# Kernel optimization log

Measured on AMD Instinct MI355X. Metric: run time of the kernel, lower is better.

Reference implementation:

```python
import jax, jax.numpy as jnp
import numpy as np

B, C, L = 8, 512, 2048


def setup_inputs() -> dict:
    key = jax.random.key(0)
    ks = jax.random.split(key, 7)
    s = 1.0 / np.sqrt(C)
    return {
        "x": jax.random.normal(ks[0], (B, C, L), dtype=jnp.float32),
        "Wq": jax.random.normal(ks[1], (C, C), dtype=jnp.float32) * s,
        "bq": jax.random.normal(ks[2], (C,), dtype=jnp.float32) * s,
        "Wk": jax.random.normal(ks[3], (C, C), dtype=jnp.float32) * s,
        "bk": jax.random.normal(ks[4], (C,), dtype=jnp.float32) * s,
        "Wv": jax.random.normal(ks[5], (C, C), dtype=jnp.float32) * s,
        "bv": jax.random.normal(ks[6], (C,), dtype=jnp.float32) * s,
    }


def reference(x, Wq, bq, Wk, bk, Wv, bv):
    # Conv1d(kernel_size=1) == per-position linear: [C_out, C_in] @ x[b,:,l]
    q = jnp.einsum('oi,bil->bol', Wq, x) + bq[None, :, None]  # [B, C, L]
    k = jnp.einsum('oi,bil->bol', Wk, x) + bk[None, :, None]
    v = jnp.einsum('oi,bil->bol', Wv, x) + bv[None, :, None]
    scale = 1.0 / jnp.sqrt(jnp.asarray(x.shape[1], dtype=x.dtype))
    # scores[b, l, m] = sum_c q[b,c,l] * k[b,c,m] / sqrt(C)
    scores = jnp.einsum('bcl,bcm->blm', q, k) * scale  # [B, L, L]
    attn = jax.nn.softmax(scores, axis=-1)
    # out[b, c, l] = sum_m v[b,c,m] * attn[b,l,m]   (== bmm(V, attn^T))
    return jnp.einsum('bcm,blm->bcl', v, attn)  # [B, C, L]
```

## Files before the change

### kernel.cpp

```cpp
#include <hip/hip_runtime.h>
#include <hip/hip_bf16.h>
#include <math.h>

#define B 8
#define C 512
#define L 2048

using bf16x8 = __bf16 __attribute__((ext_vector_type(8)));
using f32x4  = float __attribute__((ext_vector_type(4)));

#define MFMA(a, b, c) __builtin_amdgcn_mfma_f32_16x16x32_bf16((a), (b), (c), 0, 0, 0)
#define SCALE 0.044194173824159216f

__device__ __forceinline__ unsigned short f2bf(float f) {
    __hip_bfloat16 h = __float2bfloat16(f);
    return *reinterpret_cast<unsigned short*>(&h);
}
__device__ __forceinline__ void load_lds16(const unsigned short* g, unsigned short* l) {
    __builtin_amdgcn_global_load_lds(
        (const __attribute__((address_space(1))) unsigned int*)g,
        (__attribute__((address_space(3))) unsigned int*)l, 16, 0, 0);
}

template<int MODE, int KDIM>
__device__ __forceinline__ void gemm_core(
    const unsigned short* __restrict__ A,
    const unsigned short* __restrict__ Bm,
    unsigned short* As, unsigned short* Bs,
    void* __restrict__ OutV, int ldo,
    float* __restrict__ ep)
{
    const int t = threadIdx.x;
    const int wave = t >> 6, lane = t & 63;
    const int ll = t & 15, quad = (t >> 4) & 3;
    const int lr = lane >> 2, chunk = lane & 3;
    const int wm = (wave & 1) * 64, wn = (wave >> 1) * 64;

    const unsigned short* gA0 = A  + (size_t)(wave * 32 + lr) * KDIM + chunk * 8;
    const unsigned short* gB0 = Bm + (size_t)(wave * 32 + lr) * KDIM + chunk * 8;
    unsigned short* lA0 = As + (wave * 32) * 32;
    unsigned short* lB0 = Bs + (wave * 32) * 32;

    f32x4 acc[4][4];
#pragma unroll
    for (int i = 0; i < 4; ++i)
#pragma unroll
        for (int j = 0; j < 4; ++j) acc[i][j] = (f32x4){0.f, 0.f, 0.f, 0.f};

#pragma unroll 1
    for (int k0 = 0; k0 < KDIM; k0 += 32) {
        __syncthreads();
        load_lds16(gA0 + k0, lA0);
        load_lds16(gA0 + (size_t)16 * KDIM + k0, lA0 + 16 * 32);
        load_lds16(gB0 + k0, lB0);
        load_lds16(gB0 + (size_t)16 * KDIM + k0, lB0 + 16 * 32);
        __syncthreads();

        bf16x8 af[4], bf[4];
#pragma unroll
        for (int mi = 0; mi < 4; ++mi)
            af[mi] = *(const bf16x8*)&As[(wm + mi * 16 + ll) * 32 + quad * 8];
#pragma unroll
        for (int ni = 0; ni < 4; ++ni)
            bf[ni] = *(const bf16x8*)&Bs[(wn + ni * 16 + ll) * 32 + quad * 8];
#pragma unroll
        for (int mi = 0; mi < 4; ++mi)
#pragma unroll
            for (int ni = 0; ni < 4; ++ni)
                acc[mi][ni] = MFMA(af[mi], bf[ni], acc[mi][ni]);
    }

    float rpart[4][4];
    if (MODE == 2) {
#pragma unroll
        for (int mi = 0; mi < 4; ++mi)
#pragma unroll
            for (int r = 0; r < 4; ++r) rpart[mi][r] = 0.f;
    }

#pragma unroll
    for (int mi = 0; mi < 4; ++mi)
#pragma unroll
        for (int ni = 0; ni < 4; ++ni) {
            const int col = wn + ni * 16 + ll;
            float epc = 0.f;
            if (MODE == 0) epc = ep[col];
            if (MODE == 3) epc = 1.0f / ep[col];
#pragma unroll
            for (int r = 0; r < 4; ++r) {
                const int row = wm + mi * 16 + quad * 4 + r;
                float v = acc[mi][ni][r];
                if (MODE == 0)      v += epc;
                else if (MODE == 1) v += ep[row];
                else if (MODE == 2) { v = __expf(v * SCALE - 12.f); rpart[mi][r] += v; }
                else                v *= epc;
                if (MODE == 3)
                    ((float*)OutV)[(size_t)row * ldo + col] = v;
                else
                    ((unsigned short*)OutV)[(size_t)row * ldo + col] = f2bf(v);
            }
        }

    if (MODE == 2) {
#pragma unroll
        for (int mi = 0; mi < 4; ++mi)
#pragma unroll
            for (int r = 0; r < 4; ++r) {
                float s = rpart[mi][r];
                s += __shfl_xor(s, 1, 64);
                s += __shfl_xor(s, 2, 64);
                s += __shfl_xor(s, 4, 64);
                s += __shfl_xor(s, 8, 64);
                if (ll == 0) atomicAdd(ep + wm + mi * 16 + quad * 4 + r, s);
            }
    }
}

__global__ __launch_bounds__(256) void xpose_cvt(
    const float* __restrict__ x, unsigned short* __restrict__ xt)
{
    __shared__ float tile[64][69];
    const int b = blockIdx.z, l0 = blockIdx.x * 64, c0 = blockIdx.y * 64;
    const int t = threadIdx.x;
    const int lx = t & 15, cy = t >> 4;
    const float* xb = x + (size_t)b * C * L;
#pragma unroll
    for (int p = 0; p < 4; ++p) {
        float4 v = *(const float4*)(xb + (size_t)(c0 + p * 16 + cy) * L + l0 + lx * 4);
        tile[p * 16 + cy][lx * 4 + 0] = v.x;
        tile[p * 16 + cy][lx * 4 + 1] = v.y;
        tile[p * 16 + cy][lx * 4 + 2] = v.z;
        tile[p * 16 + cy][lx * 4 + 3] = v.w;
    }
    __syncthreads();
    const int ocl = t & 15, ot = t >> 4;
    unsigned short* xtb = xt + (size_t)b * L * C;
#pragma unroll
    for (int p = 0; p < 4; ++p) {
        int ol = p * 16 + ot;
        union { unsigned short h[4]; uint2 u; } pk;
#pragma unroll
        for (int i = 0; i < 4; ++i) pk.h[i] = f2bf(tile[ocl * 4 + i][ol]);
        *(uint2*)(xtb + (size_t)(l0 + ol) * C + c0 + ocl * 4) = pk.u;
    }
}

__global__ __launch_bounds__(256) void wcvt(
    const float* __restrict__ Wq, const float* __restrict__ Wk,
    const float* __restrict__ Wv, unsigned short* __restrict__ o)
{
    const int i = (blockIdx.x * 256 + threadIdx.x) * 4;
    const int which = i >> 18;
    const int off = i & 0x3FFFF;
    const float* src = (which == 0) ? Wq : (which == 1) ? Wk : Wv;
    float4 v = *(const float4*)(src + off);
    union { unsigned short h[4]; uint2 u; } pk;
    pk.h[0] = f2bf(v.x); pk.h[1] = f2bf(v.y); pk.h[2] = f2bf(v.z); pk.h[3] = f2bf(v.w);
    *(uint2*)(o + i) = pk.u;
}

__global__ __launch_bounds__(256) void qkv_gemm(
    const unsigned short* __restrict__ xt, const unsigned short* __restrict__ Wb,
    const float* __restrict__ bq, const float* __restrict__ bk,
    const float* __restrict__ bv,
    unsigned short* __restrict__ Qt, unsigned short* __restrict__ Kt,
    unsigned short* __restrict__ Vv)
{
    __shared__ unsigned short As[128 * 32], Bs[128 * 32];
    const int id = blockIdx.x;
    const int b = id & 7, r = id >> 3;
    const int which = r >> 6, tt = r & 63;
    const unsigned short* xtb = xt + (size_t)b * L * C;
    if (which < 2) {
        const int m0 = (tt & 15) * 128, n0 = (tt >> 4) * 128;
        const unsigned short* A  = xtb + (size_t)m0 * C;
        const unsigned short* Bm = Wb + (size_t)which * C * C + (size_t)n0 * C;
        unsigned short* Out = (which ? Kt : Qt) + (size_t)b * L * C
                              + (size_t)m0 * C + n0;
        gemm_core<0, C>(A, Bm, As, Bs, Out, C,
                        const_cast<float*>((which ? bk : bq) + n0));
    } else {
        const int m0 = (tt & 3) * 128, n0 = (tt >> 2) * 128;
        const unsigned short* A  = Wb + (size_t)2 * C * C + (size_t)m0 * C;
        const unsigned short* Bm = xtb + (size_t)n0 * C;
        unsigned short* Out = Vv + (size_t)b * C * L + (size_t)m0 * L + n0;
        gemm_core<1, C>(A, Bm, As, Bs, Out, L, const_cast<float*>(bv + m0));
    }
}

__global__ __launch_bounds__(256) void sc_exp(
    const unsigned short* __restrict__ Qt, const unsigned short* __restrict__ Kt,
    unsigned short* __restrict__ P, float* __restrict__ rsum,
    int hoff, int qrows, int mshift)
{
    __shared__ unsigned short As[128 * 32], Bs[128 * 32];
    const int id = blockIdx.x;
    const int b = id & 7, r = id >> 3;
    const int m0 = (r & ((1 << mshift) - 1)) * 128, n0 = (r >> mshift) * 128;
    const unsigned short* A  = Qt + (size_t)b * L * C + (size_t)(hoff + m0) * C;
    const unsigned short* Bm = Kt + (size_t)b * L * C + (size_t)n0 * C;
    unsigned short* Out = P + (size_t)b * qrows * L + (size_t)m0 * L + n0;
    float* ep = rsum + (size_t)b * L + hoff + m0;
    gemm_core<2, C>(A, Bm, As, Bs, Out, L, ep);
}

__global__ __launch_bounds__(256) void pv_gemm(
    const unsigned short* __restrict__ Vv, const unsigned short* __restrict__ P,
    const float* __restrict__ rsum, float* __restrict__ out,
    int hoff, int qrows)
{
    __shared__ unsigned short As[128 * 32], Bs[128 * 32];
    const int id = blockIdx.x;
    const int b = id & 7, r = id >> 3;
    const int m0 = (r & 3) * 128, n0 = (r >> 2) * 128;
    const unsigned short* A  = Vv + (size_t)b * C * L + (size_t)m0 * L;
    const unsigned short* Bm = P + (size_t)b * qrows * L + (size_t)n0 * L;
    float* Out = out + (size_t)b * C * L + (size_t)m0 * L + hoff + n0;
    float* ep = const_cast<float*>(rsum) + (size_t)b * L + hoff + n0;
    gemm_core<3, L>(A, Bm, As, Bs, Out, L, ep);
}

extern "C" void kernel_launch(void* const* d_in, const int* in_sizes, int n_in,
                              void* d_out, int out_size, void* d_ws, size_t ws_size,
                              hipStream_t stream) {
    const float* x  = (const float*)d_in[0];
    const float* Wq = (const float*)d_in[1];
    const float* bq = (const float*)d_in[2];
    const float* Wk = (const float*)d_in[3];
    const float* bk = (const float*)d_in[4];
    const float* Wv = (const float*)d_in[5];
    const float* bv = (const float*)d_in[6];
    float* out = (float*)d_out;

    const size_t BCL = (size_t)B * C * L;
    const bool fullP = ws_size >= 119078912ull;

    unsigned short* Qt = (unsigned short*)d_ws;
    unsigned short* Kt = Qt + BCL;
    unsigned short* Vv = Kt + BCL;
    unsigned short *Wb, *xt, *P;
    float* rsum;
    if (fullP) {
        Wb   = Vv + BCL;
        rsum = (float*)(Wb + (size_t)3 * C * C);
        xt   = (unsigned short*)(rsum + (size_t)B * L);
        P    = xt;
    } else {
        xt   = Vv + BCL;
        P    = xt;
        Wb   = P + (size_t)B * 1024 * L;
        rsum = (float*)(Wb + (size_t)3 * C * C);
    }

    hipMemsetAsync(rsum, 0, (size_t)B * L * 4, stream);
    xpose_cvt<<<dim3(L / 64, C / 64, B), 256, 0, stream>>>(x, xt);
    wcvt<<<dim3(3 * C * C / 1024), 256, 0, stream>>>(Wq, Wk, Wv, Wb);
    qkv_gemm<<<dim3(1536), 256, 0, stream>>>(xt, Wb, bq, bk, bv, Qt, Kt, Vv);

    if (fullP) {
        sc_exp<<<dim3(2048), 256, 0, stream>>>(Qt, Kt, P, rsum, 0, L, 4);
        pv_gemm<<<dim3(512), 256, 0, stream>>>(Vv, P, rsum, out, 0, L);
    } else {
        for (int h = 0; h < 2; ++h) {
            sc_exp<<<dim3(1024), 256, 0, stream>>>(Qt, Kt, P, rsum, h * 1024, 1024, 3);
            pv_gemm<<<dim3(256), 256, 0, stream>>>(Vv, P, rsum, out, h * 1024, 1024);
        }
    }
}
```

Baseline: 246.8 us.

## Fuse Q and K projections sharing A tile, fold memset into weight convert

The Q and K projection tiles now come from one block that loads the x tile once and multiplies it against both weight tiles, so there are 1024 blocks instead of 1536. The rsum zeroing moves from a separate memset into the weight-conversion kernel. The score exponent becomes exp2 with a folded scale and shift, and the bf16 conversion uses manual round-to-nearest-even bit arithmetic. Together these aim to cut redundant A-tile loads, one launch, and some epilogue ALU work. The cost is more LDS and twice the accumulator registers in the fused block, which can lower occupancy.

```diff
diff --git a/kernel.cpp b/kernel.cpp
--- a/kernel.cpp
+++ b/kernel.cpp
@@ -10,11 +10,13 @@
 using f32x4  = float __attribute__((ext_vector_type(4)));
 
 #define MFMA(a, b, c) __builtin_amdgcn_mfma_f32_16x16x32_bf16((a), (b), (c), 0, 0, 0)
-#define SCALE 0.044194173824159216f
+#define SC2 0.06375872f
+#define SH2 -17.312340f
 
 __device__ __forceinline__ unsigned short f2bf(float f) {
-    __hip_bfloat16 h = __float2bfloat16(f);
-    return *reinterpret_cast<unsigned short*>(&h);
+    unsigned int u; __builtin_memcpy(&u, &f, 4);
+    u += 0x7FFF + ((u >> 16) & 1);
+    return (unsigned short)(u >> 16);
 }
 __device__ __forceinline__ void load_lds16(const unsigned short* g, unsigned short* l) {
     __builtin_amdgcn_global_load_lds(
@@ -84,16 +86,14 @@
         for (int ni = 0; ni < 4; ++ni) {
             const int col = wn + ni * 16 + ll;
             float epc = 0.f;
-            if (MODE == 0) epc = ep[col];
             if (MODE == 3) epc = 1.0f / ep[col];
 #pragma unroll
             for (int r = 0; r < 4; ++r) {
                 const int row = wm + mi * 16 + quad * 4 + r;
                 float v = acc[mi][ni][r];
-                if (MODE == 0)      v += epc;
-                else if (MODE == 1) v += ep[row];
-                else if (MODE == 2) { v = __expf(v * SCALE - 12.f); rpart[mi][r] += v; }
-                else                v *= epc;
+                if (MODE == 1) v += ep[row];
+                else if (MODE == 2) { v = exp2f(fmaf(v, SC2, SH2)); rpart[mi][r] += v; }
+                else v *= epc;
                 if (MODE == 3)
                     ((float*)OutV)[(size_t)row * ldo + col] = v;
                 else
@@ -116,6 +116,82 @@
     }
 }
 
+__device__ __forceinline__ void qk_core(
+    const unsigned short* __restrict__ A,
+    const unsigned short* __restrict__ B0, const unsigned short* __restrict__ B1,
+    unsigned short* As, unsigned short* Bs0, unsigned short* Bs1,
+    unsigned short* O0, unsigned short* O1,
+    const float* __restrict__ ep0, const float* __restrict__ ep1)
+{
+    const int t = threadIdx.x;
+    const int wave = t >> 6, lane = t & 63;
+    const int ll = t & 15, quad = (t >> 4) & 3;
+    const int lr = lane >> 2, chunk = lane & 3;
+    const int wm = (wave & 1) * 64, wn = (wave >> 1) * 64;
+
+    const unsigned short* gA  = A  + (size_t)(wave * 32 + lr) * C + chunk * 8;
+    const unsigned short* gB0 = B0 + (size_t)(wave * 32 + lr) * C + chunk * 8;
+    const unsigned short* gB1 = B1 + (size_t)(wave * 32 + lr) * C + chunk * 8;
+    unsigned short* lA  = As  + (wave * 32) * 32;
+    unsigned short* lB0 = Bs0 + (wave * 32) * 32;
+    unsigned short* lB1 = Bs1 + (wave * 32) * 32;
+
+    f32x4 acc[2][4][4];
+#pragma unroll
+    for (int s = 0; s < 2; ++s)
+#pragma unroll
+        for (int i = 0; i < 4; ++i)
+#pragma unroll
+            for (int j = 0; j < 4; ++j) acc[s][i][j] = (f32x4){0.f, 0.f, 0.f, 0.f};
+
+#pragma unroll 1
+    for (int k0 = 0; k0 < C; k0 += 32) {
+        __syncthreads();
+        load_lds16(gA + k0, lA);
+        load_lds16(gA + (size_t)16 * C + k0, lA + 16 * 32);
+        load_lds16(gB0 + k0, lB0);
+        load_lds16(gB0 + (size_t)16 * C + k0, lB0 + 16 * 32);
+        load_lds16(gB1 + k0, lB1);
+        load_lds16(gB1 + (size_t)16 * C + k0, lB1 + 16 * 32);
+        __syncthreads();
+
+        bf16x8 af[4], bq[4], bk[4];
+#pragma unroll
+        for (int mi = 0; mi < 4; ++mi)
+            af[mi] = *(const bf16x8*)&As[(wm + mi * 16 + ll) * 32 + quad * 8];
+#pragma unroll
+        for (int ni = 0; ni < 4; ++ni) {
+            bq[ni] = *(const bf16x8*)&Bs0[(wn + ni * 16 + ll) * 32 + quad * 8];
+            bk[ni] = *(const bf16x8*)&Bs1[(wn + ni * 16 + ll) * 32 + quad * 8];
+        }
+#pragma unroll
+        for (int mi = 0; mi < 4; ++mi)
+#pragma unroll
+            for (int ni = 0; ni < 4; ++ni) {
+                acc[0][mi][ni] = MFMA(af[mi], bq[ni], acc[0][mi][ni]);
+                acc[1][mi][ni] = MFMA(af[mi], bk[ni], acc[1][mi][ni]);
+            }
+    }
+
+#pragma unroll
+    for (int s = 0; s < 2; ++s) {
+        unsigned short* O = s ? O1 : O0;
+        const float* ep = s ? ep1 : ep0;
+#pragma unroll
+        for (int mi = 0; mi < 4; ++mi)
+#pragma unroll
+            for (int ni = 0; ni < 4; ++ni) {
+                const int col = wn + ni * 16 + ll;
+                const float bias = ep[col];
+#pragma unroll
+                for (int r = 0; r < 4; ++r) {
+                    const int row = wm + mi * 16 + quad * 4 + r;
+                    O[(size_t)row * C + col] = f2bf(acc[s][mi][ni][r] + bias);
+                }
+            }
+    }
+}
+
 __global__ __launch_bounds__(256) void xpose_cvt(
     const float* __restrict__ x, unsigned short* __restrict__ xt)
 {
@@ -147,8 +223,13 @@
 
 __global__ __launch_bounds__(256) void wcvt(
     const float* __restrict__ Wq, const float* __restrict__ Wk,
-    const float* __restrict__ Wv, unsigned short* __restrict__ o)
-{
+    const float* __restrict__ Wv, unsigned short* __restrict__ o,
+    float* __restrict__ rsum)
+{
+    if (blockIdx.x < 16) {
+        float4 z = make_float4(0.f, 0.f, 0.f, 0.f);
+        *(float4*)(rsum + (blockIdx.x * 256 + threadIdx.x) * 4) = z;
+    }
     const int i = (blockIdx.x * 256 + threadIdx.x) * 4;
     const int which = i >> 18;
     const int off = i & 0x3FFFF;
@@ -166,25 +247,26 @@
     unsigned short* __restrict__ Qt, unsigned short* __restrict__ Kt,
     unsigned short* __restrict__ Vv)
 {
-    __shared__ unsigned short As[128 * 32], Bs[128 * 32];
+    __shared__ unsigned short As[128 * 32], Bs0[128 * 32], Bs1[128 * 32];
     const int id = blockIdx.x;
     const int b = id & 7, r = id >> 3;
-    const int which = r >> 6, tt = r & 63;
     const unsigned short* xtb = xt + (size_t)b * L * C;
-    if (which < 2) {
-        const int m0 = (tt & 15) * 128, n0 = (tt >> 4) * 128;
-        const unsigned short* A  = xtb + (size_t)m0 * C;
-        const unsigned short* Bm = Wb + (size_t)which * C * C + (size_t)n0 * C;
-        unsigned short* Out = (which ? Kt : Qt) + (size_t)b * L * C
-                              + (size_t)m0 * C + n0;
-        gemm_core<0, C>(A, Bm, As, Bs, Out, C,
-                        const_cast<float*>((which ? bk : bq) + n0));
+    if (r < 64) {
+        const int m0 = (r & 15) * 128, n0 = (r >> 4) * 128;
+        qk_core(xtb + (size_t)m0 * C,
+                Wb + (size_t)n0 * C,
+                Wb + (size_t)C * C + (size_t)n0 * C,
+                As, Bs0, Bs1,
+                Qt + (size_t)b * L * C + (size_t)m0 * C + n0,
+                Kt + (size_t)b * L * C + (size_t)m0 * C + n0,
+                bq + n0, bk + n0);
     } else {
-        const int m0 = (tt & 3) * 128, n0 = (tt >> 2) * 128;
+        const int rr = r - 64;
+        const int m0 = (rr & 3) * 128, n0 = (rr >> 2) * 128;
         const unsigned short* A  = Wb + (size_t)2 * C * C + (size_t)m0 * C;
         const unsigned short* Bm = xtb + (size_t)n0 * C;
         unsigned short* Out = Vv + (size_t)b * C * L + (size_t)m0 * L + n0;
-        gemm_core<1, C>(A, Bm, As, Bs, Out, L, const_cast<float*>(bv + m0));
+        gemm_core<1, C>(A, Bm, As, Bs0, Out, L, const_cast<float*>(bv + m0));
     }
 }
 
@@ -252,10 +334,9 @@
         rsum = (float*)(Wb + (size_t)3 * C * C);
     }
 
-    hipMemsetAsync(rsum, 0, (size_t)B * L * 4, stream);
     xpose_cvt<<<dim3(L / 64, C / 64, B), 256, 0, stream>>>(x, xt);
-    wcvt<<<dim3(3 * C * C / 1024), 256, 0, stream>>>(Wq, Wk, Wv, Wb);
-    qkv_gemm<<<dim3(1536), 256, 0, stream>>>(xt, Wb, bq, bk, bv, Qt, Kt, Vv);
+    wcvt<<<dim3(3 * C * C / 1024), 256, 0, stream>>>(Wq, Wk, Wv, Wb, rsum);
+    qkv_gemm<<<dim3(1024), 256, 0, stream>>>(xt, Wb, bq, bk, bv, Qt, Kt, Vv);
 
     if (fullP) {
         sc_exp<<<dim3(2048), 256, 0, stream>>>(Qt, Kt, P, rsum, 0, L, 4);
```

After: 272.2 us. 10.3% more time.
